# Kernel optimization log

Measured on AMD Instinct MI355X. Metric: run time of the kernel, lower is better.

Reference implementation:

```python
import jax, jax.numpy as jnp
import numpy as np

D_MODEL, D_FF, N_EXPERTS, TOP_K = 1024, 4096, 8, 2

def setup_inputs() -> dict:
    key = jax.random.key(0)
    k0, k1, k2, k3 = jax.random.split(key, 4)
    x = jax.random.normal(k0, (2, 2048, D_MODEL), dtype=jnp.float32)
    Wg = jax.random.normal(k1, (D_MODEL, N_EXPERTS), dtype=jnp.float32) * 0.02
    W1 = jax.random.normal(k2, (N_EXPERTS, D_MODEL, D_FF), dtype=jnp.float32) * 0.02
    b1 = jnp.zeros((N_EXPERTS, D_FF), dtype=jnp.float32)
    W2 = jax.random.normal(k3, (N_EXPERTS, D_FF, D_MODEL), dtype=jnp.float32) * 0.02
    b2 = jnp.zeros((N_EXPERTS, D_MODEL), dtype=jnp.float32)
    return {"x": x, "Wg": Wg, "W1": W1, "b1": b1, "W2": W2, "b2": b2}

def reference(x, Wg, W1, b1, W2, b2):
    B = x.shape[:-1]
    xs = x.reshape(-1, x.shape[-1])                 # [T, D]
    T = xs.shape[0]
    gate_logits = xs @ Wg                           # [T, E]
    weights, sel = jax.lax.top_k(gate_logits, TOP_K)  # [T, k]
    # softmax over the top-k logits, computed in fp32 then cast back (matches F.softmax(dtype=float).type_as)
    weights = jax.nn.softmax(weights.astype(jnp.float32), axis=1).astype(x.dtype)
    # dense all-experts MLP: [E, T, D_FF] -> [E, T, D]
    h = jax.nn.relu(jnp.einsum('td,edf->etf', xs, W1) + b1[:, None, :])
    out_e = jnp.einsum('etf,efd->etd', h, W2) + b2[:, None, :]
    # gather each token's top-k expert outputs and combine with routing weights
    tok = jnp.arange(T)
    picked = out_e[sel, tok[:, None]]               # [T, k, D]
    out = jnp.einsum('tk,tkd->td', weights, picked) # [T, D]
    return out.reshape(*B, x.shape[-1])
```

## Files before the change

kernel.cpp:

```cpp
#include <hip/hip_runtime.h>
#include <cstdint>
#include <cstddef>

#define T_TOKENS 4096
#define DM 1024
#define DF 4096
#define NE 8
#define TOPK 2
#define BK 32
#define MAX_MT 72
#define MSLOTS 8192

typedef short short8 __attribute__((ext_vector_type(8)));
typedef float f32x4 __attribute__((ext_vector_type(4)));

__device__ __forceinline__ unsigned short f2h_bits(float f) {
  _Float16 h = (_Float16)f;
  union { _Float16 h; unsigned short u; } v; v.h = h; return v.u;
}

typedef __attribute__((address_space(3))) void lds_void_t;
typedef __attribute__((address_space(1))) void gvoid_t;
__device__ __forceinline__ void gl_lds16(const void* g, void* l) {
  __builtin_amdgcn_global_load_lds((gvoid_t*)g, (lds_void_t*)l, 16, 0, 0);
}

__global__ void gate_kernel(const float* __restrict__ x, const float* __restrict__ Wg,
                            int* __restrict__ sel, float* __restrict__ wts,
                            int* __restrict__ counts, unsigned short* __restrict__ Xh) {
  int wave = threadIdx.x >> 6, lane = threadIdx.x & 63;
  int t = blockIdx.x * 4 + wave;
  const float* xr = x + (size_t)t * DM;
  unsigned short* xh = Xh + (size_t)t * DM;
  float acc[NE];
#pragma unroll
  for (int e = 0; e < NE; e++) acc[e] = 0.f;
#pragma unroll
  for (int j = 0; j < 4; j++) {
    int d4 = (lane + 64 * j) * 4;
    float4 v = *(const float4*)(xr + d4);
    ushort4 o;
    o.x = f2h_bits(v.x); o.y = f2h_bits(v.y); o.z = f2h_bits(v.z); o.w = f2h_bits(v.w);
    *(ushort4*)(xh + d4) = o;
    const float* wr = Wg + (size_t)d4 * NE;
#pragma unroll
    for (int e = 0; e < NE; e++) acc[e] += v.x * wr[e];
#pragma unroll
    for (int e = 0; e < NE; e++) acc[e] += v.y * wr[NE + e];
#pragma unroll
    for (int e = 0; e < NE; e++) acc[e] += v.z * wr[2 * NE + e];
#pragma unroll
    for (int e = 0; e < NE; e++) acc[e] += v.w * wr[3 * NE + e];
  }
#pragma unroll
  for (int e = 0; e < NE; e++) {
    float v = acc[e];
#pragma unroll
    for (int off = 32; off > 0; off >>= 1) v += __shfl_down(v, off, 64);
    acc[e] = v;
  }
  if (lane == 0) {
    int b0 = 0;
#pragma unroll
    for (int e = 1; e < NE; e++) if (acc[e] > acc[b0]) b0 = e;
    int b1 = (b0 == 0) ? 1 : 0;
#pragma unroll
    for (int e = 0; e < NE; e++) if (e != b0 && acc[e] > acc[b1]) b1 = e;
    float p = expf(acc[b1] - acc[b0]);
    float w0 = 1.f / (1.f + p);
    sel[t * 2] = b0; sel[t * 2 + 1] = b1;
    wts[t * 2] = w0; wts[t * 2 + 1] = p * w0;
    atomicAdd(&counts[b0], 1);
    atomicAdd(&counts[b1], 1);
  }
}

__global__ void scan_kernel(const int* __restrict__ counts, int* __restrict__ offsets,
                            int* __restrict__ tile_off, int* __restrict__ cursors) {
  if (threadIdx.x == 0) {
    int o = 0, to = 0;
    offsets[0] = 0; tile_off[0] = 0;
    for (int e = 0; e < NE; e++) {
      cursors[e] = o;
      o += counts[e];
      to += (counts[e] + 127) >> 7;
      offsets[e + 1] = o;
      tile_off[e + 1] = to;
    }
  }
}

__global__ void scatter_kernel(const int* __restrict__ sel, const float* __restrict__ wts,
                               int* __restrict__ cursors, int* __restrict__ rows,
                               float* __restrict__ rw, int* __restrict__ inv) {
  int t = blockIdx.x * 256 + threadIdx.x;
  if (t >= T_TOKENS) return;
#pragma unroll
  for (int k = 0; k < TOPK; k++) {
    int e = sel[t * 2 + k];
    int slot = atomicAdd(&cursors[e], 1);
    rows[slot] = t;
    rw[slot] = wts[t * 2 + k];
    inv[t * 2 + k] = slot;
  }
}

__global__ void transpose_convert(const float* __restrict__ in, unsigned short* __restrict__ outp,
                                  int R, int C) {
  __shared__ float tile[64 * 65];
  const float* inE = in + (size_t)blockIdx.z * R * C;
  unsigned short* outE = outp + (size_t)blockIdx.z * R * C;
  int c0 = blockIdx.x * 64, r0 = blockIdx.y * 64;
  int tid = threadIdx.x;
  int rr = tid >> 4, c4 = (tid & 15) * 4;
#pragma unroll
  for (int it = 0; it < 4; it++) {
    int r = rr + 16 * it;
    float4 v = *(const float4*)(inE + (size_t)(r0 + r) * C + c0 + c4);
    tile[r * 65 + c4 + 0] = v.x;
    tile[r * 65 + c4 + 1] = v.y;
    tile[r * 65 + c4 + 2] = v.z;
    tile[r * 65 + c4 + 3] = v.w;
  }
  __syncthreads();
#pragma unroll
  for (int it = 0; it < 2; it++) {
    int idx = tid + 256 * it;
    int c = idx >> 3, r8 = (idx & 7) * 8;
    short8 val;
#pragma unroll
    for (int j = 0; j < 8; j++) val[j] = (short)f2h_bits(tile[(r8 + j) * 65 + c]);
    *(short8*)(outE + (size_t)(c0 + c) * R + r0 + r8) = val;
  }
}

template <int K, int N, bool INDIR, bool SECOND, int KSPLIT>
__global__ __launch_bounds__(256, 2) void moe_gemm(
    const unsigned short* __restrict__ Aall, const unsigned short* __restrict__ Ball,
    unsigned short* __restrict__ Hout, float* __restrict__ Sout,
    const float* __restrict__ bias, const int* __restrict__ counts,
    const int* __restrict__ offsets, const int* __restrict__ tile_off,
    const int* __restrict__ rows, const float* __restrict__ rw) {
  __shared__ __align__(16) unsigned short lds[8704];
  unsigned short* ldsA = lds;
  unsigned short* ldsB = lds + 4096;

  int bx = blockIdx.x;
  int e = 0;
#pragma unroll 1
  while (e < NE && bx >= tile_off[e + 1]) e++;
  if (e >= NE) return;
  int lt = bx - tile_off[e];
  int cnt = counts[e];
  int m0 = lt * 128;
  int rowbase = offsets[e];
  int nt = blockIdx.y % (N / 128);
  int ks = blockIdx.y / (N / 128);
  int n0 = nt * 128;
  int k0 = ks * (K / KSPLIT);

  const unsigned short* Be = Ball + ((size_t)e * N + n0) * K;

  int tid = threadIdx.x;
  int lane = tid & 63, wave = tid >> 6;
  int wm = wave & 1, wn = wave >> 1;

  int rA0 = tid >> 2, rA1 = (256 + tid) >> 2, seg = tid & 3;
  int mA0 = m0 + rA0; if (mA0 >= cnt) mA0 = cnt - 1;
  int mA1 = m0 + rA1; if (mA1 >= cnt) mA1 = cnt - 1;
  size_t ia0 = INDIR ? (size_t)rows[rowbase + mA0] : (size_t)(rowbase + mA0);
  size_t ia1 = INDIR ? (size_t)rows[rowbase + mA1] : (size_t)(rowbase + mA1);
  const unsigned short* srcA0 = Aall + ia0 * K + seg * 8;
  const unsigned short* srcA1 = Aall + ia1 * K + seg * 8;
  const unsigned short* srcB0 = Be + (size_t)rA0 * K + seg * 8;
  const unsigned short* srcB1 = Be + (size_t)rA1 * K + seg * 8;
  unsigned short* dA0 = ldsA + (size_t)tid * 8;
  unsigned short* dA1 = ldsA + (size_t)(256 + tid) * 8;
  unsigned short* dB0 = ldsB + (size_t)tid * 8;
  unsigned short* dB1 = ldsB + (size_t)(256 + tid) * 8;

  f32x4 acc[4][4] = {};

  for (int kk = k0; kk < k0 + K / KSPLIT; kk += BK) {
    gl_lds16(srcA0 + kk, dA0);
    gl_lds16(srcA1 + kk, dA1);
    gl_lds16(srcB0 + kk, dB0);
    gl_lds16(srcB1 + kk, dB1);
    __syncthreads();

    short8 af[4], bfr[4];
#pragma unroll
    for (int t4 = 0; t4 < 4; t4++) {
      af[t4]  = *(const short8*)(ldsA + (wm * 64 + t4 * 16 + (lane & 15)) * BK + (lane >> 4) * 8);
      bfr[t4] = *(const short8*)(ldsB + (wn * 64 + t4 * 16 + (lane & 15)) * BK + (lane >> 4) * 8);
    }
#pragma unroll
    for (int tm = 0; tm < 4; tm++)
#pragma unroll
      for (int tn = 0; tn < 4; tn++)
        acc[tm][tn] = __builtin_amdgcn_mfma_f32_16x16x32_f16(af[tm], bfr[tn], acc[tm][tn], 0, 0, 0);
    __syncthreads();
  }

  int quad = lane >> 4, c16 = lane & 15;
  if constexpr (!SECOND) {
#pragma unroll 1
    for (int half = 0; half < 2; half++) {
      __syncthreads();
      if (wm == half) {
#pragma unroll
        for (int tm = 0; tm < 4; tm++) {
#pragma unroll
          for (int tn = 0; tn < 4; tn++) {
            int colL = wn * 64 + tn * 16 + c16;
            float b = bias[e * N + n0 + colL];
#pragma unroll
            for (int r = 0; r < 4; r++) {
              int rl = tm * 16 + quad * 4 + r;
              float v = fmaxf(acc[tm][tn][r] + b, 0.f);
              lds[rl * 136 + colL] = f2h_bits(v);
            }
          }
        }
      }
      __syncthreads();
#pragma unroll
      for (int i = 0; i < 4; i++) {
        int idx = tid + 256 * i;
        int row = idx >> 4, c8 = (idx & 15) * 8;
        int grow = m0 + half * 64 + row;
        if (grow < cnt) {
          short8 val = *(const short8*)(lds + row * 136 + c8);
          *(short8*)(Hout + (size_t)(rowbase + grow) * N + n0 + c8) = val;
        }
      }
    }
  } else {
    float* Sk = Sout + (size_t)ks * MSLOTS * N;
#pragma unroll
    for (int tm = 0; tm < 4; tm++) {
#pragma unroll
      for (int tn = 0; tn < 4; tn++) {
        int gcol = n0 + wn * 64 + tn * 16 + c16;
        float b = (ks == 0) ? bias[e * N + gcol] : 0.f;
#pragma unroll
        for (int r = 0; r < 4; r++) {
          int rl = wm * 64 + tm * 16 + quad * 4 + r;
          if (m0 + rl < cnt) {
            int slot = rowbase + m0 + rl;
            Sk[(size_t)slot * N + gcol] = (acc[tm][tn][r] + b) * rw[slot];
          }
        }
      }
    }
  }
}

__global__ void combine_kernel(const float* __restrict__ S, const int* __restrict__ inv,
                               float* __restrict__ out) {
  int wave = threadIdx.x >> 6, lane = threadIdx.x & 63;
  int t = blockIdx.x * 4 + wave;
  int s0 = inv[t * 2], s1 = inv[t * 2 + 1];
  const float4* a0 = (const float4*)(S + (size_t)s0 * DM);
  const float4* a1 = (const float4*)(S + (size_t)(MSLOTS + s0) * DM);
  const float4* b0 = (const float4*)(S + (size_t)s1 * DM);
  const float4* b1 = (const float4*)(S + (size_t)(MSLOTS + s1) * DM);
  float4* o = (float4*)(out + (size_t)t * DM);
#pragma unroll
  for (int j = 0; j < 4; j++) {
    int i = lane + 64 * j;
    float4 va = a0[i], vb = a1[i], vc = b0[i], vd = b1[i];
    float4 vo;
    vo.x = (va.x + vb.x) + (vc.x + vd.x);
    vo.y = (va.y + vb.y) + (vc.y + vd.y);
    vo.z = (va.z + vb.z) + (vc.z + vd.z);
    vo.w = (va.w + vb.w) + (vc.w + vd.w);
    o[i] = vo;
  }
}

extern "C" void kernel_launch(void* const* d_in, const int* in_sizes, int n_in,
                              void* d_out, int out_size, void* d_ws, size_t ws_size,
                              hipStream_t stream) {
  const float* x  = (const float*)d_in[0];
  const float* Wg = (const float*)d_in[1];
  const float* W1 = (const float*)d_in[2];
  const float* b1 = (const float*)d_in[3];
  const float* W2 = (const float*)d_in[4];
  const float* b2 = (const float*)d_in[5];
  float* out = (float*)d_out;

  char* ws = (char*)d_ws;
  int*   counts   = (int*)(ws + 0);
  int*   cursors  = (int*)(ws + 64);
  int*   offsets  = (int*)(ws + 128);
  int*   tile_off = (int*)(ws + 192);
  int*   sel      = (int*)(ws + 256);
  float* wts      = (float*)(ws + 33024);
  int*   rows     = (int*)(ws + 65792);
  float* rw       = (float*)(ws + 98560);
  int*   inv      = (int*)(ws + 131328);
  unsigned short* Xh  = (unsigned short*)(ws + 164096);
  unsigned short* H   = (unsigned short*)(ws + 8552704);
  unsigned short* W1t = (unsigned short*)(ws + 75661568);
  float*          S   = (float*)(ws + 75661568);
  unsigned short* W2t = (unsigned short*)(ws + 142770432);

  hipMemsetAsync(ws, 0, 128, stream);

  gate_kernel<<<T_TOKENS / 4, 256, 0, stream>>>(x, Wg, sel, wts, counts, Xh);
  scan_kernel<<<1, 64, 0, stream>>>(counts, offsets, tile_off, cursors);
  scatter_kernel<<<T_TOKENS / 256, 256, 0, stream>>>(sel, wts, cursors, rows, rw, inv);
  transpose_convert<<<dim3(DF / 64, DM / 64, NE), 256, 0, stream>>>(W1, W1t, DM, DF);
  transpose_convert<<<dim3(DM / 64, DF / 64, NE), 256, 0, stream>>>(W2, W2t, DF, DM);

  moe_gemm<DM, DF, true, false, 1><<<dim3(MAX_MT, DF / 128), 256, 0, stream>>>(
      Xh, W1t, H, nullptr, b1, counts, offsets, tile_off, rows, rw);
  moe_gemm<DF, DM, false, true, 2><<<dim3(MAX_MT, (DM / 128) * 2), 256, 0, stream>>>(
      H, W2t, nullptr, S, b2, counts, offsets, tile_off, rows, rw);

  combine_kernel<<<T_TOKENS / 4, 256, 0, stream>>>(S, inv, out);
}
```

Before: 745.5 us.

## Drop split-K in second GEMM, flatten grids, merge weight transposes, raise occupancy

```diff
diff --git a/kernel.cpp b/kernel.cpp
--- a/kernel.cpp
+++ b/kernel.cpp
@@ -105,12 +105,27 @@
   }
 }
 
-__global__ void transpose_convert(const float* __restrict__ in, unsigned short* __restrict__ outp,
-                                  int R, int C) {
+__global__ void transpose_convert(const float* __restrict__ W1, unsigned short* __restrict__ W1t,
+                                  const float* __restrict__ W2, unsigned short* __restrict__ W2t) {
   __shared__ float tile[64 * 65];
-  const float* inE = in + (size_t)blockIdx.z * R * C;
-  unsigned short* outE = outp + (size_t)blockIdx.z * R * C;
-  int c0 = blockIdx.x * 64, r0 = blockIdx.y * 64;
+  int z = blockIdx.y;
+  int R, C;
+  const float* inE;
+  unsigned short* outE;
+  int tidx = blockIdx.x;
+  int bx, by;
+  if (z < 8) {
+    R = DM; C = DF;
+    inE = W1 + (size_t)z * DM * DF;
+    outE = W1t + (size_t)z * DM * DF;
+    bx = tidx % (DF / 64); by = tidx / (DF / 64);
+  } else {
+    R = DF; C = DM;
+    inE = W2 + (size_t)(z - 8) * DM * DF;
+    outE = W2t + (size_t)(z - 8) * DM * DF;
+    bx = tidx % (DM / 64); by = tidx / (DM / 64);
+  }
+  int c0 = bx * 64, r0 = by * 64;
   int tid = threadIdx.x;
   int rr = tid >> 4, c4 = (tid & 15) * 4;
 #pragma unroll
@@ -134,8 +149,8 @@
   }
 }
 
-template <int K, int N, bool INDIR, bool SECOND, int KSPLIT>
-__global__ __launch_bounds__(256, 2) void moe_gemm(
+template <int K, int N, int NT, bool INDIR, bool SECOND>
+__global__ __launch_bounds__(256, 4) void moe_gemm(
     const unsigned short* __restrict__ Aall, const unsigned short* __restrict__ Ball,
     unsigned short* __restrict__ Hout, float* __restrict__ Sout,
     const float* __restrict__ bias, const int* __restrict__ counts,
@@ -145,7 +160,9 @@
   unsigned short* ldsA = lds;
   unsigned short* ldsB = lds + 4096;
 
-  int bx = blockIdx.x;
+  int id = blockIdx.x;
+  int nt = id % NT;
+  int bx = id / NT;
   int e = 0;
 #pragma unroll 1
   while (e < NE && bx >= tile_off[e + 1]) e++;
@@ -154,10 +171,7 @@
   int cnt = counts[e];
   int m0 = lt * 128;
   int rowbase = offsets[e];
-  int nt = blockIdx.y % (N / 128);
-  int ks = blockIdx.y / (N / 128);
   int n0 = nt * 128;
-  int k0 = ks * (K / KSPLIT);
 
   const unsigned short* Be = Ball + ((size_t)e * N + n0) * K;
 
@@ -181,7 +195,7 @@
 
   f32x4 acc[4][4] = {};
 
-  for (int kk = k0; kk < k0 + K / KSPLIT; kk += BK) {
+  for (int kk = 0; kk < K; kk += BK) {
     gl_lds16(srcA0 + kk, dA0);
     gl_lds16(srcA1 + kk, dA1);
     gl_lds16(srcB0 + kk, dB0);
@@ -236,19 +250,18 @@
       }
     }
   } else {
-    float* Sk = Sout + (size_t)ks * MSLOTS * N;
 #pragma unroll
     for (int tm = 0; tm < 4; tm++) {
 #pragma unroll
       for (int tn = 0; tn < 4; tn++) {
         int gcol = n0 + wn * 64 + tn * 16 + c16;
-        float b = (ks == 0) ? bias[e * N + gcol] : 0.f;
+        float b = bias[e * N + gcol];
 #pragma unroll
         for (int r = 0; r < 4; r++) {
           int rl = wm * 64 + tm * 16 + quad * 4 + r;
           if (m0 + rl < cnt) {
             int slot = rowbase + m0 + rl;
-            Sk[(size_t)slot * N + gcol] = (acc[tm][tn][r] + b) * rw[slot];
+            Sout[(size_t)slot * N + gcol] = (acc[tm][tn][r] + b) * rw[slot];
           }
         }
       }
@@ -261,21 +274,14 @@
   int wave = threadIdx.x >> 6, lane = threadIdx.x & 63;
   int t = blockIdx.x * 4 + wave;
   int s0 = inv[t * 2], s1 = inv[t * 2 + 1];
-  const float4* a0 = (const float4*)(S + (size_t)s0 * DM);
-  const float4* a1 = (const float4*)(S + (size_t)(MSLOTS + s0) * DM);
-  const float4* b0 = (const float4*)(S + (size_t)s1 * DM);
-  const float4* b1 = (const float4*)(S + (size_t)(MSLOTS + s1) * DM);
+  const float4* a = (const float4*)(S + (size_t)s0 * DM);
+  const float4* b = (const float4*)(S + (size_t)s1 * DM);
   float4* o = (float4*)(out + (size_t)t * DM);
 #pragma unroll
   for (int j = 0; j < 4; j++) {
-    int i = lane + 64 * j;
-    float4 va = a0[i], vb = a1[i], vc = b0[i], vd = b1[i];
-    float4 vo;
-    vo.x = (va.x + vb.x) + (vc.x + vd.x);
-    vo.y = (va.y + vb.y) + (vc.y + vd.y);
-    vo.z = (va.z + vb.z) + (vc.z + vd.z);
-    vo.w = (va.w + vb.w) + (vc.w + vd.w);
-    o[i] = vo;
+    float4 va = a[lane + 64 * j], vb = b[lane + 64 * j];
+    float4 vo; vo.x = va.x + vb.x; vo.y = va.y + vb.y; vo.z = va.z + vb.z; vo.w = va.w + vb.w;
+    o[lane + 64 * j] = vo;
   }
 }
 
@@ -311,12 +317,11 @@
   gate_kernel<<<T_TOKENS / 4, 256, 0, stream>>>(x, Wg, sel, wts, counts, Xh);
   scan_kernel<<<1, 64, 0, stream>>>(counts, offsets, tile_off, cursors);
   scatter_kernel<<<T_TOKENS / 256, 256, 0, stream>>>(sel, wts, cursors, rows, rw, inv);
-  transpose_convert<<<dim3(DF / 64, DM / 64, NE), 256, 0, stream>>>(W1, W1t, DM, DF);
-  transpose_convert<<<dim3(DM / 64, DF / 64, NE), 256, 0, stream>>>(W2, W2t, DF, DM);
-
-  moe_gemm<DM, DF, true, false, 1><<<dim3(MAX_MT, DF / 128), 256, 0, stream>>>(
+  transpose_convert<<<dim3(1024, 16), 256, 0, stream>>>(W1, W1t, W2, W2t);
+
+  moe_gemm<DM, DF, 32, true, false><<<MAX_MT * 32, 256, 0, stream>>>(
       Xh, W1t, H, nullptr, b1, counts, offsets, tile_off, rows, rw);
-  moe_gemm<DF, DM, false, true, 2><<<dim3(MAX_MT, (DM / 128) * 2), 256, 0, stream>>>(
+  moe_gemm<DF, DM, 8, false, true><<<MAX_MT * 8, 256, 0, stream>>>(
       H, W2t, nullptr, S, b2, counts, offsets, tile_off, rows, rw);
 
   combine_kernel<<<T_TOKENS / 4, 256, 0, stream>>>(S, inv, out);
```

Result: faster. 688.3 us (-7.7%).
